# Optimization experiments

Hardware: AMD Instinct MI355X
Metric: run time of the kernel (lower is better)

Reference implementation:

```python
import jax, jax.numpy as jnp
import numpy as np

B, IN, H = 16384, 512, 1024

def setup_inputs() -> dict:
    key = jax.random.key(0)
    ks = jax.random.split(key, 9)
    s_h = 1.0 / np.sqrt(H)
    s_x = 1.0 / np.sqrt(IN)
    return {
        "x": jax.random.normal(ks[0], (B, IN), jnp.float32),
        "h_prev": jax.random.normal(ks[1], (B, H), jnp.float32),
        # SLIM1 gates: Linear(H->H, bias=True)
        "W_u": jax.random.uniform(ks[2], (H, H), jnp.float32, -s_h, s_h),
        "b_u": jax.random.uniform(ks[3], (H,), jnp.float32, -s_h, s_h),
        "W_r": jax.random.uniform(ks[4], (H, H), jnp.float32, -s_h, s_h),
        "b_r": jax.random.uniform(ks[5], (H,), jnp.float32, -s_h, s_h),
        # hidden candidate: Linear(IN->H, bias=False) and Linear(H->H, bias=True)
        "W_hx": jax.random.uniform(ks[6], (H, IN), jnp.float32, -s_x, s_x),
        "W_hh": jax.random.uniform(ks[7], (H, H), jnp.float32, -s_h, s_h),
        "b_h": jax.random.uniform(ks[8], (H,), jnp.float32, -s_h, s_h),
    }

def reference(x, h_prev, W_u, b_u, W_r, b_r, W_hx, W_hh, b_h):
    # update and reset gates depend only on h_prev (SLIM1: sigmoid(W h + b))
    u = jax.nn.sigmoid(h_prev @ W_u.T + b_u)          # [B, H]
    r = jax.nn.sigmoid(h_prev @ W_r.T + b_r)          # [B, H]
    # candidate hidden state: tanh(W_hx x + W_hh (r*h) + b)
    h_cand = jnp.tanh(x @ W_hx.T + (r * h_prev) @ W_hh.T + b_h)  # [B, H]
    h_next = (1.0 - u) * h_prev + u * h_cand
    return (h_next, h_next)
```

## Files before the change

### kernel.cpp

```cpp
#include <hip/hip_runtime.h>
#include <hip/hip_bf16.h>

#define M_DIM 16384
#define IN_DIM 512
#define H_DIM 1024
#define BH (M_DIM * H_DIM)
#define K2 1536

typedef float f32x4 __attribute__((ext_vector_type(4)));
typedef short bf16x8 __attribute__((ext_vector_type(8)));

static __device__ __forceinline__ unsigned short f2bf(float f) {
    union { float f; unsigned u; } a; a.f = f;
    unsigned r = a.u + 0x7fffu + ((a.u >> 16) & 1u);
    return (unsigned short)(r >> 16);
}
static __device__ __forceinline__ float bf2f(unsigned short u) {
    union { unsigned u; float f; } a; a.u = (unsigned)u << 16;
    return a.f;
}

#define OFF_HB   0u
#define OFF_A2   16777216u
#define OFF_WU   41943040u
#define OFF_WR   42991616u
#define OFF_W2   44040192u
#define OFF_U16  45613056u
#define WS2_ELEMS 62390272u
#define WS2_NEED_BYTES (WS2_ELEMS * 2ull)

__global__ __launch_bounds__(256) void k_conv(const float* __restrict__ x,
                                              const float* __restrict__ h,
                                              const float* __restrict__ wu,
                                              const float* __restrict__ whx,
                                              const float* __restrict__ whh,
                                              const float* __restrict__ wr,
                                              unsigned short* __restrict__ ws) {
    const int total = 3604480;
    for (int u = blockIdx.x * blockDim.x + threadIdx.x; u < total;
         u += gridDim.x * blockDim.x) {
        const float* src; unsigned short* d; int lu;
        if (u < 2097152)      { lu = u;
                                src = h + (size_t)lu * 8;
                                d = ws + OFF_HB + (size_t)lu * 8; }
        else if (u < 3145728) { lu = u - 2097152;
                                src = x + (size_t)lu * 8;
                                d = ws + OFF_A2 + (size_t)(lu >> 6) * K2 + (lu & 63) * 8; }
        else if (u < 3276800) { lu = u - 3145728;
                                src = wu + (size_t)lu * 8;
                                d = ws + OFF_WU + (size_t)lu * 8; }
        else if (u < 3342336) { lu = u - 3276800;
                                src = whx + (size_t)lu * 8;
                                d = ws + OFF_W2 + (size_t)(lu >> 6) * K2 + (lu & 63) * 8; }
        else if (u < 3473408) { lu = u - 3342336;
                                src = whh + (size_t)lu * 8;
                                d = ws + OFF_W2 + (size_t)(lu >> 7) * K2 + 512 + (lu & 127) * 8; }
        else                  { lu = u - 3473408;
                                src = wr + (size_t)lu * 8;
                                d = ws + OFF_WR + (size_t)lu * 8; }
        float4 a = *reinterpret_cast<const float4*>(src);
        float4 b = *reinterpret_cast<const float4*>(src + 4);
        uint4 p;
        p.x = (unsigned)f2bf(a.x) | ((unsigned)f2bf(a.y) << 16);
        p.y = (unsigned)f2bf(a.z) | ((unsigned)f2bf(a.w) << 16);
        p.z = (unsigned)f2bf(b.x) | ((unsigned)f2bf(b.y) << 16);
        p.w = (unsigned)f2bf(b.z) | ((unsigned)f2bf(b.w) << 16);
        *reinterpret_cast<uint4*>(d) = p;
    }
}

static __device__ __forceinline__ void stage_lds(const unsigned short* __restrict__ src,
                                                 int rowBase, int ld, int ks,
                                                 unsigned short* lds, int tid) {
#pragma unroll
    for (int i = 0; i < 4; ++i) {
        int c = i * 256 + tid;
        int r = c >> 3, kc = c & 7;
        int gc = kc ^ (r & 7);
        const unsigned short* g = src + (size_t)(rowBase + r) * ld + ks + gc * 8;
        unsigned short* l = lds + c * 8;
        __builtin_amdgcn_global_load_lds((const __attribute__((address_space(1))) void*)g,
                                         (__attribute__((address_space(3))) void*)l,
                                         16, 0, 0);
    }
}

template <int KSEG>
static __device__ __forceinline__ void gemm_seg(const unsigned short* __restrict__ A, int aLd,
                                                const unsigned short* __restrict__ B, int bLd,
                                                int bm, int bn,
                                                unsigned short* As, unsigned short* Bs,
                                                int tid, int wm, int wn, int frow, int klane,
                                                f32x4 acc[4][4]) {
    for (int ks = 0; ks < KSEG; ks += 64) {
        stage_lds(A, bm * 128, aLd, ks, As, tid);
        stage_lds(B, bn * 128, bLd, ks, Bs, tid);
        __syncthreads();
#pragma unroll
        for (int kk = 0; kk < 2; ++kk) {
            bf16x8 av[4], bv[4];
#pragma unroll
            for (int m = 0; m < 4; ++m) {
                int pr = wm * 64 + m * 16 + frow;
                av[m] = *reinterpret_cast<const bf16x8*>(
                    &As[pr * 64 + (((kk << 2) + klane) ^ (pr & 7)) * 8]);
            }
#pragma unroll
            for (int n = 0; n < 4; ++n) {
                int pr = wn * 64 + n * 16 + frow;
                bv[n] = *reinterpret_cast<const bf16x8*>(
                    &Bs[pr * 64 + (((kk << 2) + klane) ^ (pr & 7)) * 8]);
            }
#pragma unroll
            for (int m = 0; m < 4; ++m)
#pragma unroll
                for (int n = 0; n < 4; ++n)
                    acc[m][n] = __builtin_amdgcn_mfma_f32_16x16x32_bf16(av[m], bv[n], acc[m][n], 0, 0, 0);
        }
        __syncthreads();
    }
}

__global__ __launch_bounds__(256, 3) void k_rgate_s(const unsigned short* __restrict__ hb,
                                                    const unsigned short* __restrict__ wrb,
                                                    const float* __restrict__ b_r,
                                                    unsigned short* __restrict__ rhA2) {
    __shared__ unsigned short As[128 * 64];
    __shared__ unsigned short Bs[128 * 64];

    int bid = blockIdx.x;
    int swz = (bid & 7) * 128 + (bid >> 3);
    int bm = swz >> 3, bn = swz & 7;

    int tid = threadIdx.x;
    int wave = tid >> 6, lane = tid & 63;
    int wm = wave >> 1, wn = wave & 1;
    int frow = lane & 15, klane = lane >> 4;

    f32x4 acc[4][4] = {};
    gemm_seg<H_DIM>(hb, H_DIM, wrb, H_DIM, bm, bn, As, Bs, tid, wm, wn, frow, klane, acc);

    int rbase = bm * 128 + wm * 64;
    int cbase = bn * 128 + wn * 64;
#pragma unroll
    for (int m = 0; m < 4; ++m) {
#pragma unroll
        for (int n = 0; n < 4; ++n) {
            int col = cbase + n * 16 + frow;
            float bs = b_r[col];
#pragma unroll
            for (int q = 0; q < 4; ++q) {
                int row = rbase + m * 16 + klane * 4 + q;
                float g = 1.0f / (1.0f + __expf(-(acc[m][n][q] + bs)));
                rhA2[(size_t)row * K2 + col] = f2bf(g * bf2f(hb[(size_t)row * H_DIM + col]));
            }
        }
    }
}

__global__ __launch_bounds__(256, 3) void k_ugate_s(const unsigned short* __restrict__ hb,
                                                    const unsigned short* __restrict__ wub,
                                                    const float* __restrict__ b_u,
                                                    unsigned short* __restrict__ u16) {
    __shared__ unsigned short As[128 * 64];
    __shared__ unsigned short Bs[128 * 64];

    int bid = blockIdx.x;
    int swz = (bid & 7) * 128 + (bid >> 3);
    int bm = swz >> 3, bn = swz & 7;

    int tid = threadIdx.x;
    int wave = tid >> 6, lane = tid & 63;
    int wm = wave >> 1, wn = wave & 1;
    int frow = lane & 15, klane = lane >> 4;

    f32x4 acc[4][4] = {};
    gemm_seg<H_DIM>(hb, H_DIM, wub, H_DIM, bm, bn, As, Bs, tid, wm, wn, frow, klane, acc);

    int rbase = bm * 128 + wm * 64;
    int cbase = bn * 128 + wn * 64;
#pragma unroll
    for (int m = 0; m < 4; ++m) {
#pragma unroll
        for (int n = 0; n < 4; ++n) {
            int col = cbase + n * 16 + frow;
            float bs = b_u[col];
#pragma unroll
            for (int q = 0; q < 4; ++q) {
                int row = rbase + m * 16 + klane * 4 + q;
                float g = 1.0f / (1.0f + __expf(-(acc[m][n][q] + bs)));
                u16[(size_t)row * H_DIM + col] = f2bf(g);
            }
        }
    }
}

__global__ __launch_bounds__(256, 3) void k_cand_b(const unsigned short* __restrict__ a2,
                                                   const unsigned short* __restrict__ w2,
                                                   const unsigned short* __restrict__ hb,
                                                   const unsigned short* __restrict__ u16,
                                                   const float* __restrict__ b_h,
                                                   float* __restrict__ out) {
    __shared__ unsigned short As[128 * 64];
    __shared__ unsigned short Bs[128 * 64];

    int bid = blockIdx.x;
    int swz = (bid & 7) * 128 + (bid >> 3);
    int bm = swz >> 3, bn = swz & 7;

    int tid = threadIdx.x;
    int wave = tid >> 6, lane = tid & 63;
    int wm = wave >> 1, wn = wave & 1;
    int frow = lane & 15, klane = lane >> 4;

    f32x4 acc[4][4] = {};
    gemm_seg<K2>(a2, K2, w2, K2, bm, bn, As, Bs, tid, wm, wn, frow, klane, acc);

    int rbase = bm * 128 + wm * 64;
    int cbase = bn * 128 + wn * 64;
#pragma unroll
    for (int m = 0; m < 4; ++m) {
#pragma unroll
        for (int n = 0; n < 4; ++n) {
            int col = cbase + n * 16 + frow;
            float bh = b_h[col];
#pragma unroll
            for (int q = 0; q < 4; ++q) {
                int row = rbase + m * 16 + klane * 4 + q;
                size_t off = (size_t)row * H_DIM + col;
                float hp = bf2f(hb[off]);
                float u = bf2f(u16[off]);
                float cpre = acc[m][n][q] + bh;
                cpre = fminf(fmaxf(cpre, -15.0f), 15.0f);
                float e = __expf(2.0f * cpre);
                float c = (e - 1.0f) / (e + 1.0f);
                float h = hp + u * (c - hp);
                out[off] = h;
                out[BH + off] = h;
            }
        }
    }
}

#define LDSS 40

static __device__ __forceinline__ void stage_f32(const float* __restrict__ src, int rowBase,
                                                 int ld, int kBase,
                                                 unsigned short* lds, int tid) {
#pragma unroll
    for (int i = 0; i < 4; ++i) {
        int idx = i * 256 + tid;
        int r = idx >> 3, c4 = idx & 7;
        const float4 v = *reinterpret_cast<const float4*>(
            src + (size_t)(rowBase + r) * ld + kBase + c4 * 4);
        uint2 p;
        p.x = (unsigned)f2bf(v.x) | ((unsigned)f2bf(v.y) << 16);
        p.y = (unsigned)f2bf(v.z) | ((unsigned)f2bf(v.w) << 16);
        *reinterpret_cast<uint2*>(lds + r * LDSS + c4 * 4) = p;
    }
}

static __device__ __forceinline__ void stage_bf16s(const unsigned short* __restrict__ src,
                                                   int rowBase, int ld, int kBase,
                                                   unsigned short* lds, int tid) {
#pragma unroll
    for (int i = 0; i < 2; ++i) {
        int idx = i * 256 + tid;
        int r = idx >> 2, c8 = idx & 3;
        const uint4 v = *reinterpret_cast<const uint4*>(
            src + (size_t)(rowBase + r) * ld + kBase + c8 * 8);
        *reinterpret_cast<uint4*>(lds + r * LDSS + c8 * 8) = v;
    }
}

__global__ __launch_bounds__(256, 2) void k_rgate(const float* __restrict__ h_prev,
                                                  const float* __restrict__ W_r,
                                                  const float* __restrict__ b_r,
                                                  unsigned short* __restrict__ rh) {
    __shared__ unsigned short As[128 * LDSS];
    __shared__ unsigned short Bs[128 * LDSS];
    int bid = blockIdx.x;
    int swz = (bid & 7) * 128 + (bid >> 3);
    int bm = swz >> 3, bn = swz & 7;
    int tid = threadIdx.x;
    int wave = tid >> 6, lane = tid & 63;
    int wm = wave >> 1, wn = wave & 1;
    int frow = lane & 15, koff = (lane >> 4) * 8;
    f32x4 acc[4][4] = {};
    for (int ks = 0; ks < H_DIM; ks += 32) {
        stage_f32(h_prev, bm * 128, H_DIM, ks, As, tid);
        stage_f32(W_r, bn * 128, H_DIM, ks, Bs, tid);
        __syncthreads();
        bf16x8 av[4], bv[4];
#pragma unroll
        for (int m = 0; m < 4; ++m)
            av[m] = *reinterpret_cast<const bf16x8*>(&As[(wm * 64 + m * 16 + frow) * LDSS + koff]);
#pragma unroll
        for (int n = 0; n < 4; ++n)
            bv[n] = *reinterpret_cast<const bf16x8*>(&Bs[(wn * 64 + n * 16 + frow) * LDSS + koff]);
#pragma unroll
        for (int m = 0; m < 4; ++m)
#pragma unroll
            for (int n = 0; n < 4; ++n)
                acc[m][n] = __builtin_amdgcn_mfma_f32_16x16x32_bf16(av[m], bv[n], acc[m][n], 0, 0, 0);
        __syncthreads();
    }
    int rbase = bm * 128 + wm * 64, cbase = bn * 128 + wn * 64;
#pragma unroll
    for (int m = 0; m < 4; ++m)
#pragma unroll
        for (int n = 0; n < 4; ++n) {
            int col = cbase + n * 16 + frow;
            float bias = b_r[col];
#pragma unroll
            for (int q = 0; q < 4; ++q) {
                int row = rbase + m * 16 + (lane >> 4) * 4 + q;
                float pre = acc[m][n][q] + bias;
                float rv = 1.0f / (1.0f + __expf(-pre));
                rh[(size_t)row * H_DIM + col] = f2bf(rv * h_prev[(size_t)row * H_DIM + col]);
            }
        }
}

__global__ __launch_bounds__(256, 2) void k_fused(const float* __restrict__ x,
                                                  const float* __restrict__ h_prev,
                                                  const float* __restrict__ W_u,
                                                  const float* __restrict__ b_u,
                                                  const float* __restrict__ W_hx,
                                                  const float* __restrict__ W_hh,
                                                  const float* __restrict__ b_h,
                                                  const unsigned short* __restrict__ rh,
                                                  float* __restrict__ out) {
    __shared__ unsigned short As[128 * LDSS];
    __shared__ unsigned short Bs[128 * LDSS];
    int bid = blockIdx.x;
    int swz = (bid & 7) * 128 + (bid >> 3);
    int bm = swz >> 3, bn = swz & 7;
    int tid = threadIdx.x;
    int wave = tid >> 6, lane = tid & 63;
    int wm = wave >> 1, wn = wave & 1;
    int frow = lane & 15, koff = (lane >> 4) * 8;
    f32x4 accu[4][4] = {};
    f32x4 accc[4][4] = {};
    for (int ks = 0; ks < H_DIM; ks += 32) {
        stage_f32(h_prev, bm * 128, H_DIM, ks, As, tid);
        stage_f32(W_u, bn * 128, H_DIM, ks, Bs, tid);
        __syncthreads();
        bf16x8 av[4], bv[4];
#pragma unroll
        for (int m = 0; m < 4; ++m)
            av[m] = *reinterpret_cast<const bf16x8*>(&As[(wm * 64 + m * 16 + frow) * LDSS + koff]);
#pragma unroll
        for (int n = 0; n < 4; ++n)
            bv[n] = *reinterpret_cast<const bf16x8*>(&Bs[(wn * 64 + n * 16 + frow) * LDSS + koff]);
#pragma unroll
        for (int m = 0; m < 4; ++m)
#pragma unroll
            for (int n = 0; n < 4; ++n)
                accu[m][n] = __builtin_amdgcn_mfma_f32_16x16x32_bf16(av[m], bv[n], accu[m][n], 0, 0, 0);
        __syncthreads();
    }
    for (int ks = 0; ks < IN_DIM; ks += 32) {
        stage_f32(x, bm * 128, IN_DIM, ks, As, tid);
        stage_f32(W_hx, bn * 128, IN_DIM, ks, Bs, tid);
        __syncthreads();
        bf16x8 av[4], bv[4];
#pragma unroll
        for (int m = 0; m < 4; ++m)
            av[m] = *reinterpret_cast<const bf16x8*>(&As[(wm * 64 + m * 16 + frow) * LDSS + koff]);
#pragma unroll
        for (int n = 0; n < 4; ++n)
            bv[n] = *reinterpret_cast<const bf16x8*>(&Bs[(wn * 64 + n * 16 + frow) * LDSS + koff]);
#pragma unroll
        for (int m = 0; m < 4; ++m)
#pragma unroll
            for (int n = 0; n < 4; ++n)
                accc[m][n] = __builtin_amdgcn_mfma_f32_16x16x32_bf16(av[m], bv[n], accc[m][n], 0, 0, 0);
        __syncthreads();
    }
    for (int ks = 0; ks < H_DIM; ks += 32) {
        stage_bf16s(rh, bm * 128, H_DIM, ks, As, tid);
        stage_f32(W_hh, bn * 128, H_DIM, ks, Bs, tid);
        __syncthreads();
        bf16x8 av[4], bv[4];
#pragma unroll
        for (int m = 0; m < 4; ++m)
            av[m] = *reinterpret_cast<const bf16x8*>(&As[(wm * 64 + m * 16 + frow) * LDSS + koff]);
#pragma unroll
        for (int n = 0; n < 4; ++n)
            bv[n] = *reinterpret_cast<const bf16x8*>(&Bs[(wn * 64 + n * 16 + frow) * LDSS + koff]);
#pragma unroll
        for (int m = 0; m < 4; ++m)
#pragma unroll
            for (int n = 0; n < 4; ++n)
                accc[m][n] = __builtin_amdgcn_mfma_f32_16x16x32_bf16(av[m], bv[n], accc[m][n], 0, 0, 0);
        __syncthreads();
    }
    int rbase = bm * 128 + wm * 64, cbase = bn * 128 + wn * 64;
#pragma unroll
    for (int m = 0; m < 4; ++m)
#pragma unroll
        for (int n = 0; n < 4; ++n) {
            int col = cbase + n * 16 + frow;
            float bu = b_u[col], bh = b_h[col];
#pragma unroll
            for (int q = 0; q < 4; ++q) {
                int row = rbase + m * 16 + (lane >> 4) * 4 + q;
                size_t off = (size_t)row * H_DIM + col;
                float hp = h_prev[off];
                float u = 1.0f / (1.0f + __expf(-(accu[m][n][q] + bu)));
                float cpre = accc[m][n][q] + bh;
                cpre = fminf(fmaxf(cpre, -15.0f), 15.0f);
                float e = __expf(2.0f * cpre);
                float c = (e - 1.0f) / (e + 1.0f);
                float h = hp + u * (c - hp);
                out[off] = h;
                out[BH + off] = h;
            }
        }
}

extern "C" void kernel_launch(void* const* d_in, const int* in_sizes, int n_in,
                              void* d_out, int out_size, void* d_ws, size_t ws_size,
                              hipStream_t stream) {
    const float* x      = (const float*)d_in[0];
    const float* h_prev = (const float*)d_in[1];
    const float* W_u    = (const float*)d_in[2];
    const float* b_u    = (const float*)d_in[3];
    const float* W_r    = (const float*)d_in[4];
    const float* b_r    = (const float*)d_in[5];
    const float* W_hx   = (const float*)d_in[6];
    const float* W_hh   = (const float*)d_in[7];
    const float* b_h    = (const float*)d_in[8];
    float* out = (float*)d_out;

    if (ws_size >= WS2_NEED_BYTES) {
        unsigned short* ws = (unsigned short*)d_ws;
        hipLaunchKernelGGL(k_conv, dim3(2048), dim3(256), 0, stream,
                           x, h_prev, W_u, W_hx, W_hh, W_r, ws);
        hipLaunchKernelGGL(k_rgate_s, dim3(1024), dim3(256), 0, stream,
                           ws + OFF_HB, ws + OFF_WR, b_r, ws + OFF_A2 + 512);
        hipLaunchKernelGGL(k_ugate_s, dim3(1024), dim3(256), 0, stream,
                           ws + OFF_HB, ws + OFF_WU, b_u, ws + OFF_U16);
        hipLaunchKernelGGL(k_cand_b, dim3(1024), dim3(256), 0, stream,
                           ws + OFF_A2, ws + OFF_W2, ws + OFF_HB, ws + OFF_U16,
                           b_h, out);
    } else {
        unsigned short* rh = (unsigned short*)d_ws;
        hipLaunchKernelGGL(k_rgate, dim3(1024), dim3(256), 0, stream, h_prev, W_r, b_r, rh);
        hipLaunchKernelGGL(k_fused, dim3(1024), dim3(256), 0, stream,
                           x, h_prev, W_u, b_u, W_hx, W_hh, b_h, rh, out);
    }
}
```

Measured before the change: 186.8 us.

## Triple-buffer LDS with interleaved async loads and 256x128 tiles in GEMM kernels

Replaces the synchronous load-then-compute GEMM loop with a three-slot LDS ring that prefetches two k-steps ahead, issuing global-to-LDS loads in chunks between MFMA groups. Block tile grows from 128x128 to 256x128 with 8 waves per block and one block per CU, and s_setprio raises priority around the MFMA bursts. The aim is to hide global load latency behind matrix math and to halve the B-tile traffic per output. In exchange, occupancy falls to one block per CU, the barriers are hand-tuned, and the vmcnt wait counts must exactly match the number of loads in flight.

```diff
diff --git a/kernel.cpp b/kernel.cpp
--- a/kernel.cpp
+++ b/kernel.cpp
@@ -69,168 +69,182 @@
     }
 }
 
-static __device__ __forceinline__ void stage_lds(const unsigned short* __restrict__ src,
-                                                 int rowBase, int ld, int ks,
-                                                 unsigned short* lds, int tid) {
-#pragma unroll
-    for (int i = 0; i < 4; ++i) {
-        int c = i * 256 + tid;
+#define SLOT_E 24576
+
+static __device__ __forceinline__ void stage_half512(const unsigned short* __restrict__ src,
+                                                     int rowBase, int ld, int ks,
+                                                     unsigned short* lds, int tid) {
+#pragma unroll
+    for (int i = 0; i < 2; ++i) {
+        int c = i * 512 + tid;
         int r = c >> 3, kc = c & 7;
         int gc = kc ^ (r & 7);
         const unsigned short* g = src + (size_t)(rowBase + r) * ld + ks + gc * 8;
-        unsigned short* l = lds + c * 8;
         __builtin_amdgcn_global_load_lds((const __attribute__((address_space(1))) void*)g,
-                                         (__attribute__((address_space(3))) void*)l,
+                                         (__attribute__((address_space(3))) void*)(lds + c * 8),
                                          16, 0, 0);
     }
 }
 
-template <int KSEG>
-static __device__ __forceinline__ void gemm_seg(const unsigned short* __restrict__ A, int aLd,
-                                                const unsigned short* __restrict__ B, int bLd,
-                                                int bm, int bn,
-                                                unsigned short* As, unsigned short* Bs,
-                                                int tid, int wm, int wn, int frow, int klane,
-                                                f32x4 acc[4][4]) {
-    for (int ks = 0; ks < KSEG; ks += 64) {
-        stage_lds(A, bm * 128, aLd, ks, As, tid);
-        stage_lds(B, bn * 128, bLd, ks, Bs, tid);
-        __syncthreads();
-#pragma unroll
-        for (int kk = 0; kk < 2; ++kk) {
-            bf16x8 av[4], bv[4];
-#pragma unroll
-            for (int m = 0; m < 4; ++m) {
-                int pr = wm * 64 + m * 16 + frow;
-                av[m] = *reinterpret_cast<const bf16x8*>(
-                    &As[pr * 64 + (((kk << 2) + klane) ^ (pr & 7)) * 8]);
-            }
-#pragma unroll
-            for (int n = 0; n < 4; ++n) {
-                int pr = wn * 64 + n * 16 + frow;
-                bv[n] = *reinterpret_cast<const bf16x8*>(
-                    &Bs[pr * 64 + (((kk << 2) + klane) ^ (pr & 7)) * 8]);
-            }
-#pragma unroll
-            for (int m = 0; m < 4; ++m)
+template <int NT>
+static __device__ __forceinline__ void gemm_pipe(const unsigned short* __restrict__ A, int aLd,
+                                                 const unsigned short* __restrict__ B, int bLd,
+                                                 int bm, int bn, unsigned short* L,
+                                                 int tid, int wm, int wn, int frow, int klane,
+                                                 f32x4 acc[4][4]) {
+    auto stage_unit = [&](int t, int u) {
+        unsigned short* slot = L + (t % 3) * SLOT_E;
+        if (u == 0)      stage_half512(A, bm * 256,       aLd, t * 64, slot,         tid);
+        else if (u == 1) stage_half512(A, bm * 256 + 128, aLd, t * 64, slot + 8192,  tid);
+        else             stage_half512(B, bn * 128,       bLd, t * 64, slot + 16384, tid);
+    };
+
+    stage_unit(0, 0); stage_unit(0, 1); stage_unit(0, 2);
+    stage_unit(1, 0); stage_unit(1, 1); stage_unit(1, 2);
+    asm volatile("s_waitcnt vmcnt(6)" ::: "memory");
+    __builtin_amdgcn_s_barrier();
+
+    for (int t = 0; t < NT; ++t) {
+        const unsigned short* base  = L + (t % 3) * SLOT_E;
+        const unsigned short* bbase = base + 16384;
+        bf16x8 bv[4][2];
+#pragma unroll
+        for (int q = 0; q < 4; ++q) {
+            if (q == 0) {
 #pragma unroll
                 for (int n = 0; n < 4; ++n)
-                    acc[m][n] = __builtin_amdgcn_mfma_f32_16x16x32_bf16(av[m], bv[n], acc[m][n], 0, 0, 0);
-        }
-        __syncthreads();
-    }
-}
-
-__global__ __launch_bounds__(256, 3) void k_rgate_s(const unsigned short* __restrict__ hb,
+#pragma unroll
+                    for (int kk = 0; kk < 2; ++kk) {
+                        int pr = wn * 64 + n * 16 + frow;
+                        bv[n][kk] = *reinterpret_cast<const bf16x8*>(
+                            &bbase[pr * 64 + (((kk << 2) + klane) ^ (pr & 7)) * 8]);
+                    }
+            }
+            bf16x8 av[2];
+#pragma unroll
+            for (int kk = 0; kk < 2; ++kk) {
+                int pr = wm * 64 + q * 16 + frow;
+                av[kk] = *reinterpret_cast<const bf16x8*>(
+                    &base[pr * 64 + (((kk << 2) + klane) ^ (pr & 7)) * 8]);
+            }
+            if (q < 3 && t + 2 < NT) stage_unit(t + 2, q);
+            __builtin_amdgcn_s_barrier();
+            __builtin_amdgcn_s_setprio(1);
+#pragma unroll
+            for (int kk = 0; kk < 2; ++kk)
+#pragma unroll
+                for (int n = 0; n < 4; ++n)
+                    acc[q][n] = __builtin_amdgcn_mfma_f32_16x16x32_bf16(av[kk], bv[n][kk], acc[q][n], 0, 0, 0);
+            __builtin_amdgcn_s_setprio(0);
+            if (q < 3) __builtin_amdgcn_s_barrier();
+        }
+        if (t < NT - 2)       { asm volatile("s_waitcnt vmcnt(6)" ::: "memory"); }
+        else if (t == NT - 2) { asm volatile("s_waitcnt vmcnt(0)" ::: "memory"); }
+        __builtin_amdgcn_s_barrier();
+    }
+}
+
+__global__ __launch_bounds__(512, 1) void k_rgate_s(const unsigned short* __restrict__ hb,
                                                     const unsigned short* __restrict__ wrb,
                                                     const float* __restrict__ b_r,
                                                     unsigned short* __restrict__ rhA2) {
-    __shared__ unsigned short As[128 * 64];
-    __shared__ unsigned short Bs[128 * 64];
-
+    __shared__ unsigned short L[3 * SLOT_E];
     int bid = blockIdx.x;
-    int swz = (bid & 7) * 128 + (bid >> 3);
+    int swz = (bid & 7) * 64 + (bid >> 3);
     int bm = swz >> 3, bn = swz & 7;
-
     int tid = threadIdx.x;
     int wave = tid >> 6, lane = tid & 63;
     int wm = wave >> 1, wn = wave & 1;
     int frow = lane & 15, klane = lane >> 4;
 
     f32x4 acc[4][4] = {};
-    gemm_seg<H_DIM>(hb, H_DIM, wrb, H_DIM, bm, bn, As, Bs, tid, wm, wn, frow, klane, acc);
-
-    int rbase = bm * 128 + wm * 64;
+    gemm_pipe<16>(hb, H_DIM, wrb, H_DIM, bm, bn, L, tid, wm, wn, frow, klane, acc);
+
+    int rbase = bm * 256 + wm * 64;
     int cbase = bn * 128 + wn * 64;
 #pragma unroll
-    for (int m = 0; m < 4; ++m) {
+    for (int q = 0; q < 4; ++q) {
 #pragma unroll
         for (int n = 0; n < 4; ++n) {
             int col = cbase + n * 16 + frow;
             float bs = b_r[col];
 #pragma unroll
-            for (int q = 0; q < 4; ++q) {
-                int row = rbase + m * 16 + klane * 4 + q;
-                float g = 1.0f / (1.0f + __expf(-(acc[m][n][q] + bs)));
+            for (int qq = 0; qq < 4; ++qq) {
+                int row = rbase + q * 16 + klane * 4 + qq;
+                float g = 1.0f / (1.0f + __expf(-(acc[q][n][qq] + bs)));
                 rhA2[(size_t)row * K2 + col] = f2bf(g * bf2f(hb[(size_t)row * H_DIM + col]));
             }
         }
     }
 }
 
-__global__ __launch_bounds__(256, 3) void k_ugate_s(const unsigned short* __restrict__ hb,
+__global__ __launch_bounds__(512, 1) void k_ugate_s(const unsigned short* __restrict__ hb,
                                                     const unsigned short* __restrict__ wub,
                                                     const float* __restrict__ b_u,
                                                     unsigned short* __restrict__ u16) {
-    __shared__ unsigned short As[128 * 64];
-    __shared__ unsigned short Bs[128 * 64];
-
+    __shared__ unsigned short L[3 * SLOT_E];
     int bid = blockIdx.x;
-    int swz = (bid & 7) * 128 + (bid >> 3);
+    int swz = (bid & 7) * 64 + (bid >> 3);
     int bm = swz >> 3, bn = swz & 7;
-
     int tid = threadIdx.x;
     int wave = tid >> 6, lane = tid & 63;
     int wm = wave >> 1, wn = wave & 1;
     int frow = lane & 15, klane = lane >> 4;
 
     f32x4 acc[4][4] = {};
-    gemm_seg<H_DIM>(hb, H_DIM, wub, H_DIM, bm, bn, As, Bs, tid, wm, wn, frow, klane, acc);
-
-    int rbase = bm * 128 + wm * 64;
+    gemm_pipe<16>(hb, H_DIM, wub, H_DIM, bm, bn, L, tid, wm, wn, frow, klane, acc);
+
+    int rbase = bm * 256 + wm * 64;
     int cbase = bn * 128 + wn * 64;
 #pragma unroll
-    for (int m = 0; m < 4; ++m) {
+    for (int q = 0; q < 4; ++q) {
 #pragma unroll
         for (int n = 0; n < 4; ++n) {
             int col = cbase + n * 16 + frow;
             float bs = b_u[col];
 #pragma unroll
-            for (int q = 0; q < 4; ++q) {
-                int row = rbase + m * 16 + klane * 4 + q;
-                float g = 1.0f / (1.0f + __expf(-(acc[m][n][q] + bs)));
+            for (int qq = 0; qq < 4; ++qq) {
+                int row = rbase + q * 16 + klane * 4 + qq;
+                float g = 1.0f / (1.0f + __expf(-(acc[q][n][qq] + bs)));
                 u16[(size_t)row * H_DIM + col] = f2bf(g);
             }
         }
     }
 }
 
-__global__ __launch_bounds__(256, 3) void k_cand_b(const unsigned short* __restrict__ a2,
+__global__ __launch_bounds__(512, 1) void k_cand_b(const unsigned short* __restrict__ a2,
                                                    const unsigned short* __restrict__ w2,
                                                    const unsigned short* __restrict__ hb,
                                                    const unsigned short* __restrict__ u16,
                                                    const float* __restrict__ b_h,
                                                    float* __restrict__ out) {
-    __shared__ unsigned short As[128 * 64];
-    __shared__ unsigned short Bs[128 * 64];
-
+    __shared__ unsigned short L[3 * SLOT_E];
     int bid = blockIdx.x;
-    int swz = (bid & 7) * 128 + (bid >> 3);
+    int swz = (bid & 7) * 64 + (bid >> 3);
     int bm = swz >> 3, bn = swz & 7;
-
     int tid = threadIdx.x;
     int wave = tid >> 6, lane = tid & 63;
     int wm = wave >> 1, wn = wave & 1;
     int frow = lane & 15, klane = lane >> 4;
 
     f32x4 acc[4][4] = {};
-    gemm_seg<K2>(a2, K2, w2, K2, bm, bn, As, Bs, tid, wm, wn, frow, klane, acc);
-
-    int rbase = bm * 128 + wm * 64;
+    gemm_pipe<24>(a2, K2, w2, K2, bm, bn, L, tid, wm, wn, frow, klane, acc);
+
+    int rbase = bm * 256 + wm * 64;
     int cbase = bn * 128 + wn * 64;
 #pragma unroll
-    for (int m = 0; m < 4; ++m) {
+    for (int q = 0; q < 4; ++q) {
 #pragma unroll
         for (int n = 0; n < 4; ++n) {
             int col = cbase + n * 16 + frow;
             float bh = b_h[col];
 #pragma unroll
-            for (int q = 0; q < 4; ++q) {
-                int row = rbase + m * 16 + klane * 4 + q;
+            for (int qq = 0; qq < 4; ++qq) {
+                int row = rbase + q * 16 + klane * 4 + qq;
                 size_t off = (size_t)row * H_DIM + col;
                 float hp = bf2f(hb[off]);
                 float u = bf2f(u16[off]);
-                float cpre = acc[m][n][q] + bh;
+                float cpre = acc[q][n][qq] + bh;
                 cpre = fminf(fmaxf(cpre, -15.0f), 15.0f);
                 float e = __expf(2.0f * cpre);
                 float c = (e - 1.0f) / (e + 1.0f);
@@ -438,11 +452,11 @@
         unsigned short* ws = (unsigned short*)d_ws;
         hipLaunchKernelGGL(k_conv, dim3(2048), dim3(256), 0, stream,
                            x, h_prev, W_u, W_hx, W_hh, W_r, ws);
-        hipLaunchKernelGGL(k_rgate_s, dim3(1024), dim3(256), 0, stream,
+        hipLaunchKernelGGL(k_rgate_s, dim3(512), dim3(512), 0, stream,
                            ws + OFF_HB, ws + OFF_WR, b_r, ws + OFF_A2 + 512);
-        hipLaunchKernelGGL(k_ugate_s, dim3(1024), dim3(256), 0, stream,
+        hipLaunchKernelGGL(k_ugate_s, dim3(512), dim3(512), 0, stream,
                            ws + OFF_HB, ws + OFF_WU, b_u, ws + OFF_U16);
-        hipLaunchKernelGGL(k_cand_b, dim3(1024), dim3(256), 0, stream,
+        hipLaunchKernelGGL(k_cand_b, dim3(512), dim3(512), 0, stream,
                            ws + OFF_A2, ws + OFF_W2, ws + OFF_HB, ws + OFF_U16,
                            b_h, out);
     } else {
```

Measured after the change: 209.9 us. +12.4%, slower.
